# Kernel optimization log

Measured on AMD Instinct MI355X. Metric: run time of the kernel, lower is better.

## Reference

```python
import jax, jax.numpy as jnp
import numpy as np

MARGIN = 1.0


def setup_inputs() -> dict:
    key = jax.random.key(0)
    k1, k2 = jax.random.split(key)
    B, C = 2048, 32000
    scores = jax.random.normal(k1, (B, C), dtype=jnp.float32)
    targets = jax.random.randint(k2, (B,), 0, C, dtype=jnp.int64)
    return {"scores": scores, "targets": targets}


def reference(scores, targets):
    B, C = scores.shape
    dt = scores.dtype
    # rank of ground-truth under descending sort (1-based), matches torch argsort(descending)+argmax
    sorted_idx = jnp.argsort(-scores, axis=-1)                      # [B, C]
    rank = jnp.argmax(sorted_idx == targets[:, None], axis=-1) + 1  # [B]
    # harmonic-number rank weights H(rank) via on-device cumulative sum of reciprocals
    harm = jnp.cumsum(1.0 / jnp.arange(1, C + 1, dtype=dt))         # [C], harm[k-1] = H(k)
    rank_weights = jax.lax.stop_gradient(harm[rank - 1])            # [B]
    # hinge loss: sum_y relu-masked (margin*1[y!=y_n] + s(x,y) - s(x,y_n))
    mask = (targets[:, None] != jnp.arange(C)[None, :]).astype(dt)  # [B, C]
    gt_scores = jnp.take_along_axis(scores, targets[:, None], axis=1)  # [B, 1]
    l = (mask * MARGIN + scores - gt_scores) * mask                 # [B, C]
    mask_pos = (l > 0).astype(dt)
    hinge = jnp.sum(l * mask_pos, axis=-1)                          # [B]
    n_pos = jnp.sum(mask_pos, axis=-1) + 1e-7                       # [B]
    loss = rank_weights / n_pos * hinge
    return jnp.mean(loss)
```

## Files before the change

kernel.cpp:

```cpp
#include <hip/hip_runtime.h>
#include <math.h>

#define B_DIM 2048
#define C_DIM 32000
#define MARGIN 1.0f
#define NTHREADS 256

typedef float vfloat4 __attribute__((ext_vector_type(4)));

__device__ __forceinline__ float waveReduceSum(float v) {
    #pragma unroll
    for (int off = 32; off > 0; off >>= 1)
        v += __shfl_down(v, off, 64);
    return v;
}

__device__ __forceinline__ void acc4(vfloat4 v, float gt, float thr,
                                     int& cntG, int& cntP, float& sumH) {
    cntG += (v.x > gt); cntG += (v.y > gt); cntG += (v.z > gt); cntG += (v.w > gt);
    float dx = v.x - thr, dy = v.y - thr, dz = v.z - thr, dw = v.w - thr;
    cntP += (dx > 0.f); cntP += (dy > 0.f); cntP += (dz > 0.f); cntP += (dw > 0.f);
    sumH += fmaxf(dx, 0.f); sumH += fmaxf(dy, 0.f);
    sumH += fmaxf(dz, 0.f); sumH += fmaxf(dw, 0.f);
}

__device__ __forceinline__ vfloat4 ntload(const vfloat4* p) {
    return __builtin_nontemporal_load(p);
}

__global__ void zero_out_kernel(float* __restrict__ out) {
    if (threadIdx.x == 0) out[0] = 0.f;
}

__global__ __launch_bounds__(NTHREADS) void row_loss_kernel(
        const float* __restrict__ scores,
        const int* __restrict__ targets,
        float* __restrict__ out) {
    const int b = blockIdx.x;
    const int tid = threadIdx.x;
    const int lane = tid & 63;
    const int wave = tid >> 6;

    const float* __restrict__ row = scores + (size_t)b * C_DIM;

    const int tgt  = targets[b];
    const float gt = row[tgt];
    const float thr = gt - MARGIN;

    int   cntG = 0;
    int   cntP = 0;
    float sumH = 0.f;

    const vfloat4* __restrict__ row4 = (const vfloat4*)row;
    const vfloat4* p = row4 + tid;
    #pragma unroll 1
    for (int k = 0; k < 3; ++k) {
        vfloat4 a0 = ntload(p);
        vfloat4 a1 = ntload(p + NTHREADS);
        vfloat4 a2 = ntload(p + 2 * NTHREADS);
        vfloat4 a3 = ntload(p + 3 * NTHREADS);
        vfloat4 a4 = ntload(p + 4 * NTHREADS);
        vfloat4 a5 = ntload(p + 5 * NTHREADS);
        vfloat4 a6 = ntload(p + 6 * NTHREADS);
        vfloat4 a7 = ntload(p + 7 * NTHREADS);
        acc4(a0, gt, thr, cntG, cntP, sumH);
        acc4(a1, gt, thr, cntG, cntP, sumH);
        acc4(a2, gt, thr, cntG, cntP, sumH);
        acc4(a3, gt, thr, cntG, cntP, sumH);
        acc4(a4, gt, thr, cntG, cntP, sumH);
        acc4(a5, gt, thr, cntG, cntP, sumH);
        acc4(a6, gt, thr, cntG, cntP, sumH);
        acc4(a7, gt, thr, cntG, cntP, sumH);
        p += 8 * NTHREADS;
    }
    {
        vfloat4 a0 = ntload(p);
        vfloat4 a1 = ntload(p + NTHREADS);
        vfloat4 a2 = ntload(p + 2 * NTHREADS);
        vfloat4 a3 = ntload(p + 3 * NTHREADS);
        vfloat4 a4 = ntload(p + 4 * NTHREADS);
        vfloat4 a5 = ntload(p + 5 * NTHREADS);
        vfloat4 a6 = ntload(p + 6 * NTHREADS);
        acc4(a0, gt, thr, cntG, cntP, sumH);
        acc4(a1, gt, thr, cntG, cntP, sumH);
        acc4(a2, gt, thr, cntG, cntP, sumH);
        acc4(a3, gt, thr, cntG, cntP, sumH);
        acc4(a4, gt, thr, cntG, cntP, sumH);
        acc4(a5, gt, thr, cntG, cntP, sumH);
        acc4(a6, gt, thr, cntG, cntP, sumH);
    }
    if (tid < 64) {
        vfloat4 a0 = ntload(row4 + 7936 + tid);
        acc4(a0, gt, thr, cntG, cntP, sumH);
    }

    float cg = waveReduceSum((float)cntG);
    float cp = waveReduceSum((float)cntP);
    float sh = waveReduceSum(sumH);

    __shared__ float red[4][3];
    if (lane == 0) { red[wave][0] = cg; red[wave][1] = cp; red[wave][2] = sh; }
    __syncthreads();

    if (tid == 0) {
        float tg = 0.f, tp = 0.f, th = 0.f;
        #pragma unroll
        for (int w = 0; w < 4; ++w) { tg += red[w][0]; tp += red[w][1]; th += red[w][2]; }
        int rank = (int)tg + 1;
        float n_pos = tp - 1.0f;
        float hinge = th - 1.0f;

        float H;
        if (rank >= 40) {
            float n = (float)rank;
            float inv = 1.0f / n;
            H = logf(n) + 0.57721566f + 0.5f * inv - (1.0f / 12.0f) * inv * inv;
        } else {
            H = 0.f;
            for (int k = 1; k <= rank; ++k) H += 1.0f / (float)k;
        }
        float loss = H / (n_pos + 1e-7f) * hinge;
        atomicAdd(out, loss * (1.0f / (float)B_DIM));
    }
}

extern "C" void kernel_launch(void* const* d_in, const int* in_sizes, int n_in,
                              void* d_out, int out_size, void* d_ws, size_t ws_size,
                              hipStream_t stream) {
    const float* scores  = (const float*)d_in[0];
    const int*   targets = (const int*)d_in[1];
    float* out = (float*)d_out;

    zero_out_kernel<<<1, 64, 0, stream>>>(out);
    row_loss_kernel<<<B_DIM, NTHREADS, 0, stream>>>(scores, targets, out);
}
```

Before: 335.1 us.

## Software-pipeline row loads with rolling buffer and simplify hinge accumulation

Replaces the batched 8-load groups with a fully unrolled rolling 8-deep register buffer, so the next load is issued as each vector is consumed and memory requests stay in flight continuously. The hinge sum is rewritten to accumulate max(v, thr) and subtract C*thr at the end, saving a subtraction per element. The zero-init kernel becomes a hipMemsetAsync. The algebraic rewrite sums large values before subtracting, which risks float cancellation error, and full unrolling raises register pressure.

```diff
diff --git a/kernel.cpp b/kernel.cpp
--- a/kernel.cpp
+++ b/kernel.cpp
@@ -16,20 +16,15 @@
 }
 
 __device__ __forceinline__ void acc4(vfloat4 v, float gt, float thr,
-                                     int& cntG, int& cntP, float& sumH) {
+                                     int& cntG, int& cntP, float& sumM) {
     cntG += (v.x > gt); cntG += (v.y > gt); cntG += (v.z > gt); cntG += (v.w > gt);
-    float dx = v.x - thr, dy = v.y - thr, dz = v.z - thr, dw = v.w - thr;
-    cntP += (dx > 0.f); cntP += (dy > 0.f); cntP += (dz > 0.f); cntP += (dw > 0.f);
-    sumH += fmaxf(dx, 0.f); sumH += fmaxf(dy, 0.f);
-    sumH += fmaxf(dz, 0.f); sumH += fmaxf(dw, 0.f);
+    cntP += (v.x > thr); cntP += (v.y > thr); cntP += (v.z > thr); cntP += (v.w > thr);
+    sumM += fmaxf(v.x, thr); sumM += fmaxf(v.y, thr);
+    sumM += fmaxf(v.z, thr); sumM += fmaxf(v.w, thr);
 }
 
 __device__ __forceinline__ vfloat4 ntload(const vfloat4* p) {
     return __builtin_nontemporal_load(p);
-}
-
-__global__ void zero_out_kernel(float* __restrict__ out) {
-    if (threadIdx.x == 0) out[0] = 0.f;
 }
 
 __global__ __launch_bounds__(NTHREADS) void row_loss_kernel(
@@ -49,66 +44,43 @@
 
     int   cntG = 0;
     int   cntP = 0;
-    float sumH = 0.f;
+    float sumM = 0.f;
 
     const vfloat4* __restrict__ row4 = (const vfloat4*)row;
-    const vfloat4* p = row4 + tid;
-    #pragma unroll 1
-    for (int k = 0; k < 3; ++k) {
-        vfloat4 a0 = ntload(p);
-        vfloat4 a1 = ntload(p + NTHREADS);
-        vfloat4 a2 = ntload(p + 2 * NTHREADS);
-        vfloat4 a3 = ntload(p + 3 * NTHREADS);
-        vfloat4 a4 = ntload(p + 4 * NTHREADS);
-        vfloat4 a5 = ntload(p + 5 * NTHREADS);
-        vfloat4 a6 = ntload(p + 6 * NTHREADS);
-        vfloat4 a7 = ntload(p + 7 * NTHREADS);
-        acc4(a0, gt, thr, cntG, cntP, sumH);
-        acc4(a1, gt, thr, cntG, cntP, sumH);
-        acc4(a2, gt, thr, cntG, cntP, sumH);
-        acc4(a3, gt, thr, cntG, cntP, sumH);
-        acc4(a4, gt, thr, cntG, cntP, sumH);
-        acc4(a5, gt, thr, cntG, cntP, sumH);
-        acc4(a6, gt, thr, cntG, cntP, sumH);
-        acc4(a7, gt, thr, cntG, cntP, sumH);
-        p += 8 * NTHREADS;
-    }
-    {
-        vfloat4 a0 = ntload(p);
-        vfloat4 a1 = ntload(p + NTHREADS);
-        vfloat4 a2 = ntload(p + 2 * NTHREADS);
-        vfloat4 a3 = ntload(p + 3 * NTHREADS);
-        vfloat4 a4 = ntload(p + 4 * NTHREADS);
-        vfloat4 a5 = ntload(p + 5 * NTHREADS);
-        vfloat4 a6 = ntload(p + 6 * NTHREADS);
-        acc4(a0, gt, thr, cntG, cntP, sumH);
-        acc4(a1, gt, thr, cntG, cntP, sumH);
-        acc4(a2, gt, thr, cntG, cntP, sumH);
-        acc4(a3, gt, thr, cntG, cntP, sumH);
-        acc4(a4, gt, thr, cntG, cntP, sumH);
-        acc4(a5, gt, thr, cntG, cntP, sumH);
-        acc4(a6, gt, thr, cntG, cntP, sumH);
+    vfloat4 buf[8];
+    #pragma unroll
+    for (int j = 0; j < 8; ++j)
+        buf[j] = ntload(row4 + tid + j * NTHREADS);
+
+    #pragma unroll
+    for (int j = 0; j < 31; ++j) {
+        vfloat4 v = buf[j & 7];
+        if (j + 8 < 31) {
+            buf[j & 7] = ntload(row4 + tid + (j + 8) * NTHREADS);
+        } else if (j + 8 == 31) {
+            if (tid < 64) buf[j & 7] = ntload(row4 + 7936 + tid);
+        }
+        acc4(v, gt, thr, cntG, cntP, sumM);
     }
     if (tid < 64) {
-        vfloat4 a0 = ntload(row4 + 7936 + tid);
-        acc4(a0, gt, thr, cntG, cntP, sumH);
+        acc4(buf[7], gt, thr, cntG, cntP, sumM);
     }
 
     float cg = waveReduceSum((float)cntG);
     float cp = waveReduceSum((float)cntP);
-    float sh = waveReduceSum(sumH);
+    float sm = waveReduceSum(sumM);
 
     __shared__ float red[4][3];
-    if (lane == 0) { red[wave][0] = cg; red[wave][1] = cp; red[wave][2] = sh; }
+    if (lane == 0) { red[wave][0] = cg; red[wave][1] = cp; red[wave][2] = sm; }
     __syncthreads();
 
     if (tid == 0) {
-        float tg = 0.f, tp = 0.f, th = 0.f;
+        float tg = 0.f, tp = 0.f, tm = 0.f;
         #pragma unroll
-        for (int w = 0; w < 4; ++w) { tg += red[w][0]; tp += red[w][1]; th += red[w][2]; }
+        for (int w = 0; w < 4; ++w) { tg += red[w][0]; tp += red[w][1]; tm += red[w][2]; }
         int rank = (int)tg + 1;
         float n_pos = tp - 1.0f;
-        float hinge = th - 1.0f;
+        float hinge = (tm - (float)C_DIM * thr) - 1.0f;
 
         float H;
         if (rank >= 40) {
@@ -131,6 +103,6 @@
     const int*   targets = (const int*)d_in[1];
     float* out = (float*)d_out;
 
-    zero_out_kernel<<<1, 64, 0, stream>>>(out);
+    hipMemsetAsync(out, 0, sizeof(float), stream);
     row_loss_kernel<<<B_DIM, NTHREADS, 0, stream>>>(scores, targets, out);
 }
```

Result: no change. 333.1 us (-0.6%).
